# Kernel optimization log

Hardware: AMD Instinct MI355X
Metric: run time of the kernel (lower is better)

Reference implementation:

```python
import jax, jax.numpy as jnp
import numpy as np

EPS = 1e-5

def layer_norm(x, w, b):
    mu = jnp.mean(x, axis=-1, keepdims=True)
    var = jnp.var(x, axis=-1, keepdims=True)
    return (x - mu) * jax.lax.rsqrt(var + EPS) * w + b

def setup_inputs() -> dict:
    key = jax.random.key(0)
    ks = jax.random.split(key, 9)
    B, N, d, hidden = 1, 512, 64, 128
    s = 0.02
    return {
        "z": jax.random.normal(ks[0], (B, N, N, d), dtype=jnp.float32),
        "ln_in_w": jnp.ones((d,), jnp.float32),
        "ln_in_b": jnp.zeros((d,), jnp.float32),
        "Wp": jax.random.normal(ks[1], (d, 2 * hidden), jnp.float32) * s,
        "Wg": jax.random.normal(ks[2], (d, 2 * hidden), jnp.float32) * s,
        "ln_out_w": jnp.ones((hidden,), jnp.float32),
        "ln_out_b": jnp.zeros((hidden,), jnp.float32),
        "Wout": jax.random.normal(ks[3], (hidden, d), jnp.float32) * s,
        "Wgate": jax.random.normal(ks[4], (d, d), jnp.float32) * s,
    }

def reference(z, ln_in_w, ln_in_b, Wp, Wg, ln_out_w, ln_out_b, Wout, Wgate):
    # z: [B, N, N, d]
    h = layer_norm(z, ln_in_w, ln_in_b)
    p = h @ Wp                               # [B,N,N,2*hidden]
    g_in = jax.nn.sigmoid(h @ Wg)            # [B,N,N,2*hidden]
    pg = p * g_in
    a, b = jnp.split(pg, 2, axis=-1)         # each [B,N,N,hidden]
    # direction == 'outgoing'
    out = jnp.einsum('bikd,bjkd->bijd', a, b)  # [B,N,N,hidden]
    out = layer_norm(out, ln_out_w, ln_out_b)
    g_out = jax.nn.sigmoid(h @ Wgate)        # [B,N,N,d]
    return (out @ Wout) * g_out              # [B,N,N,d]
```

## Files before the change

### kernel.cpp

```cpp
#include <hip/hip_runtime.h>
#include <hip/hip_fp16.h>


typedef _Float16 half_t;
typedef _Float16 f16x4 __attribute__((ext_vector_type(4)));
typedef _Float16 f16x8 __attribute__((ext_vector_type(8)));
typedef float f32x4 __attribute__((ext_vector_type(4)));

#define NSEQ 512
#define HID 128
#define ROWS (NSEQ * NSEQ)

#define GLOAD16(src, dst)                                                        \
    __builtin_amdgcn_global_load_lds(                                            \
        (const __attribute__((address_space(1))) void*)(src),                    \
        (__attribute__((address_space(3))) void*)(dst), 16, 0, 0)

__device__ __forceinline__ float fast_sigmoid(float x) {
    float e = __builtin_amdgcn_exp2f(-1.44269504088896f * x);
    return __builtin_amdgcn_rcpf(1.f + e);
}

__global__ void k_prep_w(const float* __restrict__ Wp, const float* __restrict__ Wg,
                         const float* __restrict__ Wgate,
                         const float* __restrict__ ln_out_w, const float* __restrict__ ln_out_b,
                         const float* __restrict__ Wout,
                         half_t* __restrict__ Wimg, half_t* __restrict__ W1t,
                         float* __restrict__ s1, float* __restrict__ s2) {
    int bid = blockIdx.x, t = threadIdx.x;
    if (bid < 18) {
        int chunk = bid * 256 + t;
        int ch = chunk >= 2304;
        int q = chunk - ch * 2304;
        int lr = q >> 3, slot = q & 7;
        int co = slot ^ (lr & 7);
        int grow;
        if (lr < 128)      grow = ch * 128 + lr;
        else if (lr < 256) grow = 256 + ch * 128 + (lr - 128);
        else               grow = 512 + ch * 32 + (lr - 256);
        f16x8 vals;
        #pragma unroll
        for (int j = 0; j < 8; ++j) {
            int l = co * 8 + j;
            float v;
            if (grow < 256)      v = Wp[l * 256 + grow];
            else if (grow < 512) v = Wg[l * 256 + (grow - 256)];
            else                 v = Wgate[l * 64 + (grow - 512)];
            vals[j] = (half_t)v;
        }
        *(f16x8*)(Wimg + (size_t)chunk * 8) = vals;
    } else {
        #pragma unroll
        for (int i = 0; i < 32; ++i) {
            int idx = t * 32 + i;
            int o = idx >> 7, c = idx & 127;
            W1t[idx] = (half_t)(ln_out_w[c] * Wout[c * 64 + o]);
        }
        if (t < 64) {
            float a1 = 0.f, a2 = 0.f;
            for (int c = 0; c < 128; ++c) {
                float wo = Wout[c * 64 + t];
                a1 += ln_out_w[c] * wo;
                a2 += ln_out_b[c] * wo;
            }
            s1[t] = a1; s2[t] = a2;
        }
    }
}

__global__ __launch_bounds__(256) void k_ln_in(const float* __restrict__ z,
                                               const float* __restrict__ w,
                                               const float* __restrict__ b,
                                               half_t* __restrict__ h) {
    int t = threadIdx.x;
    int row = blockIdx.x * 16 + (t >> 4);
    int c4 = t & 15;
    f32x4 x = *(const f32x4*)(z + (size_t)row * 64 + c4 * 4);
    float s = x[0] + x[1] + x[2] + x[3];
    float s2 = x[0]*x[0] + x[1]*x[1] + x[2]*x[2] + x[3]*x[3];
    #pragma unroll
    for (int off = 1; off < 16; off <<= 1) {
        s  += __shfl_xor(s,  off, 64);
        s2 += __shfl_xor(s2, off, 64);
    }
    float mu = s * (1.f / 64.f);
    float var = s2 * (1.f / 64.f) - mu * mu;
    float rs = rsqrtf(var + 1e-5f);
    f32x4 wv = *(const f32x4*)(w + c4 * 4);
    f32x4 bv = *(const f32x4*)(b + c4 * 4);
    f16x4 o;
    #pragma unroll
    for (int j = 0; j < 4; ++j)
        o[j] = (half_t)((x[j] - mu) * rs * wv[j] + bv[j]);
    *(f16x4*)(h + (size_t)row * 64 + c4 * 4) = o;
}

__global__ __launch_bounds__(256) void k_proj(const half_t* __restrict__ h,
                                              const half_t* __restrict__ Wimg,
                                              half_t* __restrict__ a_t,
                                              half_t* __restrict__ b_t,
                                              half_t* __restrict__ g_out) {
    __shared__ half_t Wl[288 * 64];
    __shared__ half_t pgl[64 * 66];

    int t = threadIdx.x;
    int ch = blockIdx.y;
    int bx = blockIdx.x;
    int r0 = bx * 64;
    int wid = t >> 6, lane = t & 63;
    int m = lane & 15, g = lane >> 4;

    const half_t* wsrc = Wimg + (size_t)ch * 2304 * 8;
    #pragma unroll
    for (int it = 0; it < 9; ++it) {
        int cb = it * 256 + wid * 64;
        GLOAD16(wsrc + (size_t)(cb + lane) * 8, Wl + (size_t)cb * 8);
    }

    int growbase = r0 + wid * 16;
    f16x8 af[2];
    #pragma unroll
    for (int ks = 0; ks < 2; ++ks)
        af[ks] = *(const f16x8*)(h + (size_t)(growbase + m) * 64 + ks * 32 + g * 8);

    __syncthreads();

    half_t* dst = (ch == 0) ? a_t : b_t;
    int swz = (bx >> 4) & 3;

    for (int grp = 0; grp < 2; ++grp) {
        #pragma unroll
        for (int pt4 = 0; pt4 < 4; ++pt4) {
            int pt = grp * 4 + pt4;
            f32x4 accp = {0.f, 0.f, 0.f, 0.f}, accg = {0.f, 0.f, 0.f, 0.f};
            #pragma unroll
            for (int ks = 0; ks < 2; ++ks) {
                int kb = (ks * 32 + g * 8) * 2;
                int lrp = pt * 16 + m;
                f16x8 bp = *(const f16x8*)((char*)Wl + lrp * 128 + (kb ^ ((lrp & 7) << 4)));
                int lrg = 128 + pt * 16 + m;
                f16x8 bg = *(const f16x8*)((char*)Wl + lrg * 128 + (kb ^ ((lrg & 7) << 4)));
                accp = __builtin_amdgcn_mfma_f32_16x16x32_f16(af[ks], bp, accp, 0, 0, 0);
                accg = __builtin_amdgcn_mfma_f32_16x16x32_f16(af[ks], bg, accg, 0, 0, 0);
            }
            f16x4 pk;
            #pragma unroll
            for (int r = 0; r < 4; ++r)
                pk[r] = (half_t)(accp[r] * fast_sigmoid(accg[r]));
            *(f16x4*)&pgl[(pt4 * 16 + m) * 66 + wid * 16 + g * 4] = pk;
        }
        __syncthreads();
        #pragma unroll
        for (int it = 0; it < 2; ++it) {
            int chunk = it * 256 + t;
            int cl = chunk >> 3, r8 = chunk & 7;
            f16x8 v = *(const f16x8*)&pgl[cl * 66 + r8 * 8];
            int dk = (r8 & 4) | ((r8 & 3) ^ swz);
            *(f16x8*)(dst + (size_t)(grp * 64 + cl) * ROWS + r0 + dk * 8) = v;
        }
        __syncthreads();
    }

    for (int gt = 0; gt < 2; ++gt) {
        f32x4 acc = {0.f, 0.f, 0.f, 0.f};
        #pragma unroll
        for (int ks = 0; ks < 2; ++ks) {
            int kb = (ks * 32 + g * 8) * 2;
            int lr = 256 + gt * 16 + m;
            f16x8 bb = *(const f16x8*)((char*)Wl + lr * 128 + (kb ^ ((lr & 7) << 4)));
            acc = __builtin_amdgcn_mfma_f32_16x16x32_f16(af[ks], bb, acc, 0, 0, 0);
        }
        int och = ch * 32 + gt * 16 + m;
        #pragma unroll
        for (int r = 0; r < 4; ++r) {
            float og = fast_sigmoid(acc[r]);
            int grow = growbase + g * 4 + r;
            g_out[(size_t)grow * 64 + och] = (half_t)og;
        }
    }
}

__global__ __launch_bounds__(512) void k_einsum(const half_t* __restrict__ a_t,
                                                const half_t* __restrict__ b_t,
                                                half_t* __restrict__ out_mid) {
    __shared__ half_t Al[2][256 * 32];
    __shared__ half_t Bl[2][256 * 32];

    int t = threadIdx.x;
    int bid = blockIdx.x;
    int xcd = bid & 7, kk = bid >> 3;
    int c = xcd + 8 * (kk >> 2);
    int tt = kk & 3;
    int i0 = (tt & 1) * 256, j0 = (tt >> 1) * 256;

    const half_t* A = a_t + (size_t)c * ROWS;
    const half_t* B = b_t + (size_t)c * ROWS;

    int wid = t >> 6, lane = t & 63;
    int m = lane & 15, g = lane >> 4;
    int wr = wid >> 2, wc = wid & 3;

    f32x4 acc[8][4] = {};

#define STAGE(ktt, Ab, Bb)                                                        \
    {                                                                             \
        _Pragma("unroll")                                                         \
        for (int rnd = 0; rnd < 2; ++rnd) {                                       \
            int cb = rnd * 512 + wid * 64;           \
            int chunk = cb + lane;                                                \
            int row = chunk >> 2, slot = chunk & 3;                               \
            GLOAD16(A + (size_t)(i0 + row) * 512 + (ktt) * 32 + slot * 8,         \
                    (Ab) + (size_t)cb * 8);                                       \
            GLOAD16(B + (size_t)(j0 + row) * 512 + (ktt) * 32 + slot * 8,         \
                    (Bb) + (size_t)cb * 8);                                       \
        }                                                                         \
    }

    STAGE(0, Al[0], Bl[0]);

    #pragma unroll 2
    for (int kt = 0; kt < 16; ++kt) {
        const int cur = kt & 1;
        if (kt < 15) {
            STAGE(kt + 1, Al[cur ^ 1], Bl[cur ^ 1]);
            asm volatile("s_waitcnt vmcnt(4)" ::: "memory");
        } else {
            asm volatile("s_waitcnt vmcnt(0)" ::: "memory");
        }
        __builtin_amdgcn_s_barrier();
        __builtin_amdgcn_sched_barrier(0);

        const half_t* Ac = Al[cur];
        const half_t* Bc = Bl[cur];
        f16x8 bf[4];
        #pragma unroll
        for (int ni = 0; ni < 4; ++ni) {
            int lrow = wc * 64 + ni * 16 + m;
            int so = (g ^ ((lrow >> 1) & 3)) * 16;
            bf[ni] = *(const f16x8*)((char*)Bc + lrow * 64 + so);
        }
        #pragma unroll
        for (int mi = 0; mi < 8; ++mi) {
            int lrow = wr * 128 + mi * 16 + m;
            int so = (g ^ ((lrow >> 1) & 3)) * 16;
            f16x8 afr = *(const f16x8*)((char*)Ac + lrow * 64 + so);
            #pragma unroll
            for (int ni = 0; ni < 4; ++ni)
                acc[mi][ni] = __builtin_amdgcn_mfma_f32_16x16x32_f16(afr, bf[ni], acc[mi][ni], 0, 0, 0);
        }
        __builtin_amdgcn_s_barrier();
    }
#undef STAGE

    half_t* O = out_mid + (size_t)c * ROWS;
    #pragma unroll
    for (int mi = 0; mi < 8; ++mi) {
        #pragma unroll
        for (int ni = 0; ni < 4; ++ni) {
            int row = i0 + wr * 128 + mi * 16 + g * 4;
            int col = j0 + wc * 64 + ni * 16 + m;
            #pragma unroll
            for (int r = 0; r < 4; ++r)
                O[(size_t)(row + r) * 512 + col] = (half_t)acc[mi][ni][r];
        }
    }
}

__global__ __launch_bounds__(256) void k_final(const half_t* __restrict__ out_mid,
                                               const half_t* __restrict__ W1t,
                                               const float* __restrict__ s1g,
                                               const float* __restrict__ s2g,
                                               const half_t* __restrict__ g_out,
                                               float* __restrict__ out) {
    __shared__ half_t midl[128 * 64];
    __shared__ half_t midt[64 * 128];
    __shared__ half_t w1l[64 * 128];
    __shared__ half_t gl[64 * 72];
    __shared__ float smu[64], srs[64], s1l[64], s2l[64];

    int t = threadIdx.x;
    int pos0 = blockIdx.x * 64;

    #pragma unroll
    for (int it = 0; it < 4; ++it) {
        int chunk = it * 256 + t;
        int cc = chunk >> 3, co = chunk & 7;
        *(uint4*)((char*)midl + cc * 128 + co * 16) =
            *(const uint4*)(out_mid + (size_t)cc * ROWS + pos0 + co * 8);
    }
    #pragma unroll
    for (int it = 0; it < 4; ++it) {
        int chunk = it * 256 + t;
        int row = chunk >> 4, slot = chunk & 15;
        *(uint4*)((char*)w1l + row * 256 + ((slot * 16) ^ ((row & 7) << 4))) =
            *(const uint4*)(W1t + row * 128 + slot * 8);
    }
    #pragma unroll
    for (int it = 0; it < 2; ++it) {
        int chunk = it * 256 + t;
        int row = chunk >> 3, co = chunk & 7;
        *(uint4*)((char*)gl + row * 144 + co * 16) =
            *(const uint4*)(g_out + (size_t)(pos0 + row) * 64 + co * 8);
    }
    if (t < 64) { s1l[t] = s1g[t]; s2l[t] = s2g[t]; }
    __syncthreads();

    {
        int p = t >> 2, q = t & 3;
        float s = 0.f, s2 = 0.f;
        #pragma unroll
        for (int cc4 = 0; cc4 < 4; ++cc4) {
            f16x8 pack;
            #pragma unroll
            for (int j = 0; j < 8; ++j) {
                half_t hv = midl[(q * 32 + cc4 * 8 + j) * 64 + p];
                float v = (float)hv;
                s += v; s2 += v * v;
                pack[j] = hv;
            }
            int slot = q * 4 + cc4;
            *(f16x8*)((char*)midt + p * 256 + ((slot * 16) ^ ((p & 7) << 4))) = pack;
        }
        s  += __shfl_xor(s, 1, 64);  s  += __shfl_xor(s, 2, 64);
        s2 += __shfl_xor(s2, 1, 64); s2 += __shfl_xor(s2, 2, 64);
        if (q == 0) {
            float mu = s * (1.f / 128.f);
            float var = s2 * (1.f / 128.f) - mu * mu;
            smu[p] = mu;
            srs[p] = rsqrtf(var + 1e-5f);
        }
    }
    __syncthreads();

    int wid = t >> 6, lane = t & 63;
    int m = lane & 15, g = lane >> 4;

    f32x4 acc[4] = {};
    #pragma unroll
    for (int ks = 0; ks < 4; ++ks) {
        int arow = wid * 16 + m;
        f16x8 af = *(const f16x8*)((char*)midt + arow * 256 +
                                   (((4 * ks + g) * 16) ^ ((arow & 7) << 4)));
        #pragma unroll
        for (int ni = 0; ni < 4; ++ni) {
            int brow = ni * 16 + m;
            f16x8 bf = *(const f16x8*)((char*)w1l + brow * 256 +
                                       (((4 * ks + g) * 16) ^ ((brow & 7) << 4)));
            acc[ni] = __builtin_amdgcn_mfma_f32_16x16x32_f16(af, bf, acc[ni], 0, 0, 0);
        }
    }

    #pragma unroll
    for (int ni = 0; ni < 4; ++ni) {
        int o = ni * 16 + m;
        float v1 = s1l[o], v2 = s2l[o];
        #pragma unroll
        for (int r = 0; r < 4; ++r) {
            int lrow = wid * 16 + g * 4 + r;
            float mu = smu[lrow], rs = srs[lrow];
            float val = acc[ni][r] * rs - mu * rs * v1 + v2;
            float gate = (float)gl[lrow * 72 + o];
            out[(size_t)(pos0 + lrow) * 64 + o] = val * gate;
        }
    }
}

extern "C" void kernel_launch(void* const* d_in, const int* in_sizes, int n_in,
                              void* d_out, int out_size, void* d_ws, size_t ws_size,
                              hipStream_t stream) {
    const float* z        = (const float*)d_in[0];
    const float* ln_in_w  = (const float*)d_in[1];
    const float* ln_in_b  = (const float*)d_in[2];
    const float* Wp       = (const float*)d_in[3];
    const float* Wg       = (const float*)d_in[4];
    const float* ln_out_w = (const float*)d_in[5];
    const float* ln_out_b = (const float*)d_in[6];
    const float* Wout     = (const float*)d_in[7];
    const float* Wgate    = (const float*)d_in[8];
    float* out = (float*)d_out;

    char* wsb = (char*)d_ws;
    half_t* Wimg = (half_t*)wsb;
    half_t* W1t  = (half_t*)(wsb + 81920);
    float*  s1   = (float*)(wsb + 98304);
    float*  s2   = (float*)(wsb + 98560);
    half_t* a_t  = (half_t*)(wsb + 131072);
    half_t* b_t  = a_t + (size_t)HID * ROWS;
    half_t* gout = b_t + (size_t)HID * ROWS;
    half_t* omid = gout + (size_t)ROWS * 64;
    half_t* h    = omid;

    k_prep_w<<<dim3(19), dim3(256), 0, stream>>>(Wp, Wg, Wgate, ln_out_w, ln_out_b, Wout,
                                                 Wimg, W1t, s1, s2);
    k_ln_in<<<dim3(ROWS / 16), dim3(256), 0, stream>>>(z, ln_in_w, ln_in_b, h);
    k_proj<<<dim3(ROWS / 64, 2), dim3(256), 0, stream>>>(h, Wimg, a_t, b_t, gout);
    k_einsum<<<dim3(512), dim3(512), 0, stream>>>(a_t, b_t, omid);
    k_final<<<dim3(ROWS / 64), dim3(256), 0, stream>>>(omid, W1t, s1, s2, gout, out);
}
```

Baseline: 161.4 us.

## Fuse input layernorm into projection kernel and triple-buffer einsum loads

Removes the separate k_ln_in kernel: k_proj now reads fp32 z directly, computes per-row mean and variance with cross-lane shuffles, and builds the fp16 MFMA operands in registers. This drops the half-precision h round-trip through global memory and one launch. The projection block grows to 512 threads covering 128 rows, with a wider staging buffer and an adjusted swizzle for the a/b transposed stores. The einsum kernel moves from double to triple buffering with a two-tile lookahead, which raises LDS usage and may reduce occupancy. Because each block now reads z directly, z is read twice overall, once per channel block.

```diff
diff --git a/kernel.cpp b/kernel.cpp
--- a/kernel.cpp
+++ b/kernel.cpp
@@ -68,65 +68,67 @@
     }
 }
 
-__global__ __launch_bounds__(256) void k_ln_in(const float* __restrict__ z,
-                                               const float* __restrict__ w,
-                                               const float* __restrict__ b,
-                                               half_t* __restrict__ h) {
-    int t = threadIdx.x;
-    int row = blockIdx.x * 16 + (t >> 4);
-    int c4 = t & 15;
-    f32x4 x = *(const f32x4*)(z + (size_t)row * 64 + c4 * 4);
-    float s = x[0] + x[1] + x[2] + x[3];
-    float s2 = x[0]*x[0] + x[1]*x[1] + x[2]*x[2] + x[3]*x[3];
-    #pragma unroll
-    for (int off = 1; off < 16; off <<= 1) {
-        s  += __shfl_xor(s,  off, 64);
-        s2 += __shfl_xor(s2, off, 64);
-    }
-    float mu = s * (1.f / 64.f);
-    float var = s2 * (1.f / 64.f) - mu * mu;
-    float rs = rsqrtf(var + 1e-5f);
-    f32x4 wv = *(const f32x4*)(w + c4 * 4);
-    f32x4 bv = *(const f32x4*)(b + c4 * 4);
-    f16x4 o;
-    #pragma unroll
-    for (int j = 0; j < 4; ++j)
-        o[j] = (half_t)((x[j] - mu) * rs * wv[j] + bv[j]);
-    *(f16x4*)(h + (size_t)row * 64 + c4 * 4) = o;
-}
-
-__global__ __launch_bounds__(256) void k_proj(const half_t* __restrict__ h,
+__global__ __launch_bounds__(512) void k_proj(const float* __restrict__ z,
+                                              const float* __restrict__ lnw,
+                                              const float* __restrict__ lnb,
                                               const half_t* __restrict__ Wimg,
                                               half_t* __restrict__ a_t,
                                               half_t* __restrict__ b_t,
                                               half_t* __restrict__ g_out) {
     __shared__ half_t Wl[288 * 64];
-    __shared__ half_t pgl[64 * 66];
+    __shared__ half_t pgl[64 * 130];
 
     int t = threadIdx.x;
     int ch = blockIdx.y;
     int bx = blockIdx.x;
-    int r0 = bx * 64;
+    int r0 = bx * 128;
     int wid = t >> 6, lane = t & 63;
     int m = lane & 15, g = lane >> 4;
 
     const half_t* wsrc = Wimg + (size_t)ch * 2304 * 8;
     #pragma unroll
-    for (int it = 0; it < 9; ++it) {
-        int cb = it * 256 + wid * 64;
-        GLOAD16(wsrc + (size_t)(cb + lane) * 8, Wl + (size_t)cb * 8);
+    for (int it = 0; it < 5; ++it) {
+        int cb = it * 512 + wid * 64;
+        if (cb < 2304)
+            GLOAD16(wsrc + (size_t)(cb + lane) * 8, Wl + (size_t)cb * 8);
     }
 
     int growbase = r0 + wid * 16;
+    int p = growbase + m;
+    f32x4 zv[4];
+    #pragma unroll
+    for (int ks = 0; ks < 2; ++ks) {
+        zv[ks * 2]     = *(const f32x4*)(z + (size_t)p * 64 + ks * 32 + g * 8);
+        zv[ks * 2 + 1] = *(const f32x4*)(z + (size_t)p * 64 + ks * 32 + g * 8 + 4);
+    }
+    float s = 0.f, s2 = 0.f;
+    #pragma unroll
+    for (int q = 0; q < 4; ++q)
+        #pragma unroll
+        for (int j = 0; j < 4; ++j) { float v = zv[q][j]; s += v; s2 += v * v; }
+    s  += __shfl_xor(s, 16, 64);  s2 += __shfl_xor(s2, 16, 64);
+    s  += __shfl_xor(s, 32, 64);  s2 += __shfl_xor(s2, 32, 64);
+    float mu = s * (1.f / 64.f);
+    float var = s2 * (1.f / 64.f) - mu * mu;
+    float rs = rsqrtf(var + 1e-5f);
     f16x8 af[2];
     #pragma unroll
-    for (int ks = 0; ks < 2; ++ks)
-        af[ks] = *(const f16x8*)(h + (size_t)(growbase + m) * 64 + ks * 32 + g * 8);
+    for (int ks = 0; ks < 2; ++ks) {
+        f32x4 w0 = *(const f32x4*)(lnw + ks * 32 + g * 8);
+        f32x4 w1 = *(const f32x4*)(lnw + ks * 32 + g * 8 + 4);
+        f32x4 b0 = *(const f32x4*)(lnb + ks * 32 + g * 8);
+        f32x4 b1 = *(const f32x4*)(lnb + ks * 32 + g * 8 + 4);
+        #pragma unroll
+        for (int j = 0; j < 4; ++j) {
+            af[ks][j]     = (half_t)((zv[ks * 2][j]     - mu) * rs * w0[j] + b0[j]);
+            af[ks][4 + j] = (half_t)((zv[ks * 2 + 1][j] - mu) * rs * w1[j] + b1[j]);
+        }
+    }
 
     __syncthreads();
 
     half_t* dst = (ch == 0) ? a_t : b_t;
-    int swz = (bx >> 4) & 3;
+    int swz = (bx >> 3) & 3;
 
     for (int grp = 0; grp < 2; ++grp) {
         #pragma unroll
@@ -147,15 +149,15 @@
             #pragma unroll
             for (int r = 0; r < 4; ++r)
                 pk[r] = (half_t)(accp[r] * fast_sigmoid(accg[r]));
-            *(f16x4*)&pgl[(pt4 * 16 + m) * 66 + wid * 16 + g * 4] = pk;
+            *(f16x4*)&pgl[(pt4 * 16 + m) * 130 + wid * 16 + g * 4] = pk;
         }
         __syncthreads();
         #pragma unroll
         for (int it = 0; it < 2; ++it) {
-            int chunk = it * 256 + t;
-            int cl = chunk >> 3, r8 = chunk & 7;
-            f16x8 v = *(const f16x8*)&pgl[cl * 66 + r8 * 8];
-            int dk = (r8 & 4) | ((r8 & 3) ^ swz);
+            int chunk = it * 512 + t;
+            int cl = chunk >> 4, r16 = chunk & 15;
+            f16x8 v = *(const f16x8*)&pgl[cl * 130 + r16 * 8];
+            int dk = (r16 & 12) | ((r16 & 3) ^ swz);
             *(f16x8*)(dst + (size_t)(grp * 64 + cl) * ROWS + r0 + dk * 8) = v;
         }
         __syncthreads();
@@ -183,8 +185,8 @@
 __global__ __launch_bounds__(512) void k_einsum(const half_t* __restrict__ a_t,
                                                 const half_t* __restrict__ b_t,
                                                 half_t* __restrict__ out_mid) {
-    __shared__ half_t Al[2][256 * 32];
-    __shared__ half_t Bl[2][256 * 32];
+    __shared__ half_t Al[3][256 * 32];
+    __shared__ half_t Bl[3][256 * 32];
 
     int t = threadIdx.x;
     int bid = blockIdx.x;
@@ -217,12 +219,15 @@
     }
 
     STAGE(0, Al[0], Bl[0]);
-
-    #pragma unroll 2
+    STAGE(1, Al[1], Bl[1]);
+
+    int cur = 0;
     for (int kt = 0; kt < 16; ++kt) {
-        const int cur = kt & 1;
-        if (kt < 15) {
-            STAGE(kt + 1, Al[cur ^ 1], Bl[cur ^ 1]);
+        if (kt < 14) {
+            int nb = cur + 2; if (nb >= 3) nb -= 3;
+            STAGE(kt + 2, Al[nb], Bl[nb]);
+            asm volatile("s_waitcnt vmcnt(8)" ::: "memory");
+        } else if (kt == 14) {
             asm volatile("s_waitcnt vmcnt(4)" ::: "memory");
         } else {
             asm volatile("s_waitcnt vmcnt(0)" ::: "memory");
@@ -249,6 +254,7 @@
                 acc[mi][ni] = __builtin_amdgcn_mfma_f32_16x16x32_f16(afr, bf[ni], acc[mi][ni], 0, 0, 0);
         }
         __builtin_amdgcn_s_barrier();
+        cur = (cur == 2) ? 0 : cur + 1;
     }
 #undef STAGE
 
@@ -388,12 +394,11 @@
     half_t* b_t  = a_t + (size_t)HID * ROWS;
     half_t* gout = b_t + (size_t)HID * ROWS;
     half_t* omid = gout + (size_t)ROWS * 64;
-    half_t* h    = omid;
 
     k_prep_w<<<dim3(19), dim3(256), 0, stream>>>(Wp, Wg, Wgate, ln_out_w, ln_out_b, Wout,
                                                  Wimg, W1t, s1, s2);
-    k_ln_in<<<dim3(ROWS / 16), dim3(256), 0, stream>>>(z, ln_in_w, ln_in_b, h);
-    k_proj<<<dim3(ROWS / 64, 2), dim3(256), 0, stream>>>(h, Wimg, a_t, b_t, gout);
+    k_proj<<<dim3(ROWS / 128, 2), dim3(512), 0, stream>>>(z, ln_in_w, ln_in_b, Wimg,
+                                                          a_t, b_t, gout);
     k_einsum<<<dim3(512), dim3(512), 0, stream>>>(a_t, b_t, omid);
     k_final<<<dim3(ROWS / 64), dim3(256), 0, stream>>>(omid, W1t, s1, s2, gout, out);
 }
```

New measurement: 182.5 us. 1.13x slower.

## Give each einsum wave private LDS tiles with triple-buffered barrier-free loads

Applied to the files above, without the earlier changes.

Restructures the batched einsum so every wave loads its own 128x64 A/B tiles into a private LDS region, with a three-stage prefetch pipeline and no workgroup barriers. Blocks shrink to 256 threads and the grid doubles. This removes barrier stalls and deepens latency hiding. In exchange, A and B rows that were shared across waves are now loaded redundantly, which raises global and L2 traffic.

```diff
diff --git a/kernel.cpp b/kernel.cpp
--- a/kernel.cpp
+++ b/kernel.cpp
@@ -180,75 +180,80 @@
     }
 }
 
-__global__ __launch_bounds__(512) void k_einsum(const half_t* __restrict__ a_t,
+__global__ __launch_bounds__(256) void k_einsum(const half_t* __restrict__ a_t,
                                                 const half_t* __restrict__ b_t,
                                                 half_t* __restrict__ out_mid) {
-    __shared__ half_t Al[2][256 * 32];
-    __shared__ half_t Bl[2][256 * 32];
+    __shared__ half_t lds[4][3][6144];
 
     int t = threadIdx.x;
+    int wid = t >> 6, lane = t & 63;
+    int m = lane & 15, g = lane >> 4;
+
     int bid = blockIdx.x;
-    int xcd = bid & 7, kk = bid >> 3;
-    int c = xcd + 8 * (kk >> 2);
-    int tt = kk & 3;
-    int i0 = (tt & 1) * 256, j0 = (tt >> 1) * 256;
+    int xcd = bid & 7;
+    int r = bid >> 3;
+    int tt = r & 7, u = r >> 3;
+    int c = xcd + 8 * u;
+    int id = tt * 4 + wid;
+    int i0 = (id >> 3) * 128, j0 = (id & 7) * 64;
 
     const half_t* A = a_t + (size_t)c * ROWS;
     const half_t* B = b_t + (size_t)c * ROWS;
 
-    int wid = t >> 6, lane = t & 63;
-    int m = lane & 15, g = lane >> 4;
-    int wr = wid >> 2, wc = wid & 3;
-
     f32x4 acc[8][4] = {};
 
-#define STAGE(ktt, Ab, Bb)                                                        \
+#define STAGE(ktt, bi)                                                            \
     {                                                                             \
+        half_t* dA = &lds[wid][bi][0];                                            \
+        half_t* dB = &lds[wid][bi][4096];                                         \
         _Pragma("unroll")                                                         \
-        for (int rnd = 0; rnd < 2; ++rnd) {                                       \
-            int cb = rnd * 512 + wid * 64;           \
-            int chunk = cb + lane;                                                \
-            int row = chunk >> 2, slot = chunk & 3;                               \
-            GLOAD16(A + (size_t)(i0 + row) * 512 + (ktt) * 32 + slot * 8,         \
-                    (Ab) + (size_t)cb * 8);                                       \
-            GLOAD16(B + (size_t)(j0 + row) * 512 + (ktt) * 32 + slot * 8,         \
-                    (Bb) + (size_t)cb * 8);                                       \
+        for (int inst = 0; inst < 8; ++inst) {                                    \
+            int q = inst * 64 + lane;                                             \
+            GLOAD16(A + (size_t)(i0 + (q >> 2)) * 512 + (ktt) * 32 + (q & 3) * 8, \
+                    dA + (size_t)inst * 512);                                     \
         }                                                                         \
-    }
-
-    STAGE(0, Al[0], Bl[0]);
-
-    #pragma unroll 2
+        _Pragma("unroll")                                                         \
+        for (int inst = 0; inst < 4; ++inst) {                                    \
+            int q = inst * 64 + lane;                                             \
+            GLOAD16(B + (size_t)(j0 + (q >> 2)) * 512 + (ktt) * 32 + (q & 3) * 8, \
+                    dB + (size_t)inst * 512);                                     \
+        }                                                                         \
+    }
+
+    STAGE(0, 0);
+    STAGE(1, 1);
+
+    #pragma unroll
     for (int kt = 0; kt < 16; ++kt) {
-        const int cur = kt & 1;
-        if (kt < 15) {
-            STAGE(kt + 1, Al[cur ^ 1], Bl[cur ^ 1]);
-            asm volatile("s_waitcnt vmcnt(4)" ::: "memory");
+        const int cur = kt % 3;
+        if (kt < 14) {
+            STAGE(kt + 2, (kt + 2) % 3);
+            asm volatile("s_waitcnt vmcnt(24)" ::: "memory");
+        } else if (kt == 14) {
+            asm volatile("s_waitcnt vmcnt(12)" ::: "memory");
         } else {
             asm volatile("s_waitcnt vmcnt(0)" ::: "memory");
         }
-        __builtin_amdgcn_s_barrier();
         __builtin_amdgcn_sched_barrier(0);
 
-        const half_t* Ac = Al[cur];
-        const half_t* Bc = Bl[cur];
+        const half_t* Ac = &lds[wid][cur][0];
+        const half_t* Bc = &lds[wid][cur][4096];
         f16x8 bf[4];
         #pragma unroll
         for (int ni = 0; ni < 4; ++ni) {
-            int lrow = wc * 64 + ni * 16 + m;
-            int so = (g ^ ((lrow >> 1) & 3)) * 16;
-            bf[ni] = *(const f16x8*)((char*)Bc + lrow * 64 + so);
+            int lrow = ni * 16 + m;
+            bf[ni] = *(const f16x8*)((const char*)Bc + lrow * 64 +
+                                     ((g ^ ((lrow >> 1) & 3)) << 4));
         }
         #pragma unroll
         for (int mi = 0; mi < 8; ++mi) {
-            int lrow = wr * 128 + mi * 16 + m;
-            int so = (g ^ ((lrow >> 1) & 3)) * 16;
-            f16x8 afr = *(const f16x8*)((char*)Ac + lrow * 64 + so);
+            int lrow = mi * 16 + m;
+            f16x8 afr = *(const f16x8*)((const char*)Ac + lrow * 64 +
+                                        ((g ^ ((lrow >> 1) & 3)) << 4));
             #pragma unroll
             for (int ni = 0; ni < 4; ++ni)
                 acc[mi][ni] = __builtin_amdgcn_mfma_f32_16x16x32_f16(afr, bf[ni], acc[mi][ni], 0, 0, 0);
         }
-        __builtin_amdgcn_s_barrier();
     }
 #undef STAGE
 
@@ -257,11 +262,11 @@
     for (int mi = 0; mi < 8; ++mi) {
         #pragma unroll
         for (int ni = 0; ni < 4; ++ni) {
-            int row = i0 + wr * 128 + mi * 16 + g * 4;
-            int col = j0 + wc * 64 + ni * 16 + m;
+            int row = i0 + mi * 16 + g * 4;
+            int col = j0 + ni * 16 + m;
             #pragma unroll
-            for (int r = 0; r < 4; ++r)
-                O[(size_t)(row + r) * 512 + col] = (half_t)acc[mi][ni][r];
+            for (int r2 = 0; r2 < 4; ++r2)
+                O[(size_t)(row + r2) * 512 + col] = (half_t)acc[mi][ni][r2];
         }
     }
 }
@@ -394,6 +399,6 @@
                                                  Wimg, W1t, s1, s2);
     k_ln_in<<<dim3(ROWS / 16), dim3(256), 0, stream>>>(z, ln_in_w, ln_in_b, h);
     k_proj<<<dim3(ROWS / 64, 2), dim3(256), 0, stream>>>(h, Wimg, a_t, b_t, gout);
-    k_einsum<<<dim3(512), dim3(512), 0, stream>>>(a_t, b_t, omid);
+    k_einsum<<<dim3(1024), dim3(256), 0, stream>>>(a_t, b_t, omid);
     k_final<<<dim3(ROWS / 64), dim3(256), 0, stream>>>(omid, W1t, s1, s2, gout, out);
 }
```

Result: slower. 167.1 us (+3.5%).
